# Kernel optimization log

Measured on AMD Instinct MI355X. Metric: run time of the kernel, lower is better.

Reference implementation:

```python
import jax, jax.numpy as jnp
import numpy as np

# MSDeformAttn-style fusion config (canonical deformable-DETR defaults)
D = 256      # d_model
NH = 8       # n_heads
NP = 4       # n_points per level
NL = 2       # n_levels (= num_feature_levels: modality v and modality i)
B, H, W = 4, 64, 64


def setup_inputs() -> dict:
    key = jax.random.key(0)
    ks = jax.random.split(key, 8)
    s = 0.02
    return {
        'input_v': jax.random.normal(ks[0], (B, D, H, W), jnp.float32),
        'input_i': jax.random.normal(ks[1], (B, D, H, W), jnp.float32),
        'W_value': jax.random.normal(ks[2], (D, D), jnp.float32) * s,
        'b_value': jnp.zeros((D,), jnp.float32),
        'W_off':   jax.random.normal(ks[3], (D, NH * NL * NP * 2), jnp.float32) * s,
        'b_off':   jax.random.normal(ks[4], (NH * NL * NP * 2,), jnp.float32) * s,
        'W_attn':  jax.random.normal(ks[5], (D, NH * NL * NP), jnp.float32) * s,
        'b_attn':  jnp.zeros((NH * NL * NP,), jnp.float32),
        'W_out':   jax.random.normal(ks[6], (D, D), jnp.float32) * s,
        'b_out':   jnp.zeros((D,), jnp.float32),
    }


def _bilinear_sample(value_l, locs, Hl, Wl):
    # value_l: (B, NH, HW, dh)  flattened per-level value
    # locs:    (B, Lq, NH, NP, 2) normalized sampling locations in [0,1]
    # returns  (B, NH, Lq, NP, dh); grid_sample semantics: zeros padding, align_corners=False
    b, nh, hw, dh = value_l.shape
    lq = locs.shape[1]
    x = locs[..., 0] * Wl - 0.5
    y = locs[..., 1] * Hl - 0.5
    x0 = jnp.floor(x)
    y0 = jnp.floor(y)
    dx = x - x0
    dy = y - y0
    x0i = x0.astype(jnp.int32)
    y0i = y0.astype(jnp.int32)
    out = jnp.zeros((b, nh, lq, NP, dh), value_l.dtype)
    corners = [
        (x0i,     y0i,     (1 - dx) * (1 - dy)),
        (x0i + 1, y0i,     dx * (1 - dy)),
        (x0i,     y0i + 1, (1 - dx) * dy),
        (x0i + 1, y0i + 1, dx * dy),
    ]
    for xi, yi, wgt in corners:
        valid = ((xi >= 0) & (xi < Wl) & (yi >= 0) & (yi < Hl)).astype(value_l.dtype)
        idx = jnp.clip(yi, 0, Hl - 1) * Wl + jnp.clip(xi, 0, Wl - 1)      # (B,Lq,NH,NP)
        idx_t = idx.transpose(0, 2, 1, 3).reshape(b, nh, lq * NP, 1)       # (B,NH,Lq*NP,1)
        g = jnp.take_along_axis(value_l, idx_t, axis=2)                    # (B,NH,Lq*NP,dh)
        g = g.reshape(b, nh, lq, NP, dh)
        w_t = (wgt * valid).transpose(0, 2, 1, 3)[..., None]               # (B,NH,Lq,NP,1)
        out = out + g * w_t
    return out


def reference(input_v, input_i, W_value, b_value, W_off, b_off, W_attn, b_attn, W_out, b_out):
    b, c, h, w = input_v.shape
    hw = h * w
    lq = NL * hw
    dh = c // NH

    # flatten both modalities into one token sequence (level 0 = v, level 1 = i)
    src_v = input_v.reshape(b, c, hw).transpose(0, 2, 1)
    src_i = input_i.reshape(b, c, hw).transpose(0, 2, 1)
    src = jnp.concatenate([src_v, src_i], axis=1)                          # (B, Lq, C)

    value = (src @ W_value + b_value).reshape(b, lq, NH, dh)
    value = value.transpose(0, 2, 1, 3)                                    # (B, NH, Lq, dh)
    value_levels = [value[:, :, :hw], value[:, :, hw:]]

    offsets = (src @ W_off + b_off).reshape(b, lq, NH, NL, NP, 2)
    attn = jax.nn.softmax((src @ W_attn + b_attn).reshape(b, lq, NH, NL * NP), axis=-1)
    attn = attn.reshape(b, lq, NH, NL, NP)

    # reference points: normalized pixel centers, same grid for both levels
    xs = (jnp.arange(w, dtype=jnp.float32) + 0.5) / w
    ys = (jnp.arange(h, dtype=jnp.float32) + 0.5) / h
    gy, gx = jnp.meshgrid(ys, xs, indexing='ij')
    ref = jnp.stack([gx.reshape(-1), gy.reshape(-1)], axis=-1)             # (HW, 2)
    ref = jnp.concatenate([ref, ref], axis=0)                              # (Lq, 2)

    norm = jnp.array([w, h], dtype=jnp.float32)
    locs = ref[None, :, None, None, None, :] + offsets / norm              # (B,Lq,NH,NL,NP,2)

    sampled = jnp.stack(
        [_bilinear_sample(value_levels[l], locs[:, :, :, l], h, w) for l in range(NL)],
        axis=3)                                                            # (B,NH,Lq,NL,NP,dh)

    fused = jnp.einsum('bqhlp,bhqlpd->bqhd', attn, sampled).reshape(b, lq, c)
    out = fused @ W_out + b_out                                            # (B, Lq, C)

    out_v = out[:, :hw]
    out_i = out[:, hw:]
    o = out_v + out_i                                                      # (B, HW, C)
    return o.transpose(0, 2, 1).reshape(b, c, h, w)
```

## Files before the change

### kernel.cpp

```cpp
#include <hip/hip_runtime.h>

#define HW 4096
#define LQ 8192
#define DD 256

typedef __bf16 bf16x8 __attribute__((ext_vector_type(8)));
typedef float  f32x4  __attribute__((ext_vector_type(4)));
typedef unsigned int u32;
typedef u32 u32x4 __attribute__((ext_vector_type(4)));
typedef u32 u32x2 __attribute__((ext_vector_type(2)));

__device__ __forceinline__ float bflo(u32 u) { return __uint_as_float(u << 16); }
__device__ __forceinline__ float bfhi(u32 u) { return __uint_as_float(u & 0xffff0000u); }

#define GLOAD16(g, l) __builtin_amdgcn_global_load_lds(                     \
    (__attribute__((address_space(1))) void*)(g),                          \
    (__attribute__((address_space(3))) void*)(l), 16, 0, 0)

__global__ __launch_bounds__(256) void prep_all(const float* __restrict__ in_v,
                                                const float* __restrict__ in_i,
                                                const float* __restrict__ Wv,
                                                const float* __restrict__ Wo,
                                                const float* __restrict__ Wa,
                                                const float* __restrict__ Wout,
                                                char* __restrict__ srcS,
                                                char* __restrict__ WcatT,
                                                char* __restrict__ WoutT)
{
    __shared__ float tile[64][68];
    if (blockIdx.z < 8) {
        const int q0 = blockIdx.x * 64;
        const int k0 = blockIdx.y * 64;
        const int bz = blockIdx.z;
        const float* src = ((bz & 1) ? in_i : in_v) + (size_t)(bz >> 1) * (DD * HW);
        const int t  = threadIdx.x;
        const int ql = (t & 15) * 4;
        const int kl = t >> 4;
#pragma unroll
        for (int rr = 0; rr < 4; ++rr) {
            const float4 v = *(const float4*)(src + (size_t)(k0 + kl + rr * 16) * HW + q0 + ql);
            *(float4*)&tile[kl + rr * 16][ql] = v;
        }
        __syncthreads();
        const int qrow = t >> 2;
        const int kc   = (t & 3) * 16;
        const int row  = (bz >> 1) * LQ + (bz & 1) * HW + q0 + qrow;
        bf16x8 p0, p1;
#pragma unroll
        for (int j = 0; j < 8; ++j) {
            p0[j] = (__bf16)tile[kc + j][qrow];
            p1[j] = (__bf16)tile[kc + 8 + j][qrow];
        }
        char* drow = srcS + (size_t)row * 512;
        const int sw   = (row & 7) << 4;
        const int base = k0 * 2 + kc * 2;
        *(bf16x8*)(drow + ((base)      ^ sw)) = p0;
        *(bf16x8*)(drow + ((base + 16) ^ sw)) = p1;
    } else {
        const int flat = blockIdx.y * 64 + blockIdx.x;
        if (flat >= 120) return;
        const int gi = flat * 256 + threadIdx.x;
        if (gi < 448 * 32) {
            const int row = gi >> 5;
            const int g   = gi & 31;
            const int k   = g * 8;
            const float* col; int stride;
            if (row < 256)      { col = Wv + row;         stride = 256; }
            else if (row < 384) { col = Wo + (row - 256); stride = 128; }
            else                { col = Wa + (row - 384); stride = 64;  }
            bf16x8 p;
#pragma unroll
            for (int j = 0; j < 8; ++j) p[j] = (__bf16)col[(size_t)(k + j) * stride];
            char* d = WcatT + (size_t)row * 512;
            *(bf16x8*)(d + ((g * 16) ^ ((row & 7) << 4))) = p;
        } else {
            const int gj = gi - 448 * 32;
            if (gj >= 256 * 64) return;
            const int c = gj >> 6;
            const int g = gj & 63;
            const int k = (g * 8) & 255;
            bf16x8 p;
#pragma unroll
            for (int j = 0; j < 8; ++j) p[j] = (__bf16)Wout[(size_t)(k + j) * 256 + c];
            char* d = WoutT + (size_t)c * 1024;
            *(bf16x8*)(d + ((g * 16) ^ ((c & 7) << 4))) = p;
        }
    }
}

__global__ __launch_bounds__(256) void mfma_proj(const char* __restrict__ srcS,
                                                 const char* __restrict__ WcatT,
                                                 const float* __restrict__ b_value,
                                                 const float* __restrict__ b_off,
                                                 const float* __restrict__ b_attn,
                                                 __bf16* __restrict__ valueB,
                                                 __bf16* __restrict__ offB,
                                                 __bf16* __restrict__ attnB)
{
    __shared__ char smem[24576];
    char* As = smem;
    char* Bs = smem + 16384;

    const int M0 = blockIdx.x * 128;
    const int N0 = blockIdx.y * 64;
    const int t = threadIdx.x;
    const int w = t >> 6;
    const int l = t & 63;
    const int lm = l & 15, lk = l >> 4;
    const int wave_m = (w >> 1) * 64;
    const int wave_n = (w & 1) * 32;

    f32x4 acc[4][2] = {};

    const char* Ab = As + (wave_m + lm) * 128;
    const char* Bb = Bs + (wave_n + lm) * 128;
    const int go0 = (lk ^ (l & 7)) * 16;
    const int go1 = go0 ^ 64;

    for (int kt = 0; kt < 4; ++kt) {
        __syncthreads();
        const int kb = kt * 128;
#pragma unroll
        for (int c = 0; c < 4; ++c) {
            const char* g = srcS + (size_t)(M0 + w * 32 + c * 8 + (l >> 3)) * 512 + kb + (l & 7) * 16;
            GLOAD16(g, As + (w * 4 + c) * 1024);
        }
#pragma unroll
        for (int c = 0; c < 2; ++c) {
            const char* g = WcatT + (size_t)(N0 + w * 16 + c * 8 + (l >> 3)) * 512 + kb + (l & 7) * 16;
            GLOAD16(g, Bs + (w * 2 + c) * 1024);
        }
        __syncthreads();

        bf16x8 af[4], bb[2];
#pragma unroll
        for (int mi = 0; mi < 4; ++mi) af[mi] = *(const bf16x8*)(Ab + mi * 2048 + go0);
#pragma unroll
        for (int ni = 0; ni < 2; ++ni) bb[ni] = *(const bf16x8*)(Bb + ni * 2048 + go0);
#pragma unroll
        for (int mi = 0; mi < 4; ++mi)
#pragma unroll
            for (int ni = 0; ni < 2; ++ni)
                acc[mi][ni] = __builtin_amdgcn_mfma_f32_16x16x32_bf16(af[mi], bb[ni], acc[mi][ni], 0, 0, 0);
#pragma unroll
        for (int mi = 0; mi < 4; ++mi) af[mi] = *(const bf16x8*)(Ab + mi * 2048 + go1);
#pragma unroll
        for (int ni = 0; ni < 2; ++ni) bb[ni] = *(const bf16x8*)(Bb + ni * 2048 + go1);
#pragma unroll
        for (int mi = 0; mi < 4; ++mi)
#pragma unroll
            for (int ni = 0; ni < 2; ++ni)
                acc[mi][ni] = __builtin_amdgcn_mfma_f32_16x16x32_bf16(af[mi], bb[ni], acc[mi][ni], 0, 0, 0);
    }

    if (N0 < 256) {
#pragma unroll
        for (int ni = 0; ni < 2; ++ni) {
            const int cl = N0 + wave_n + ni * 16 + lm;
            const float bv = b_value[cl];
#pragma unroll
            for (int mi = 0; mi < 4; ++mi) {
                const int row = M0 + wave_m + mi * 16 + lk * 4;
#pragma unroll
                for (int r = 0; r < 4; ++r)
                    valueB[(size_t)(row + r) * 256 + cl] = (__bf16)(acc[mi][ni][r] + bv);
            }
        }
    } else if (N0 < 384) {
#pragma unroll
        for (int ni = 0; ni < 2; ++ni) {
            const int cl = (N0 - 256) + wave_n + ni * 16 + lm;
            const float bv = b_off[cl];
#pragma unroll
            for (int mi = 0; mi < 4; ++mi) {
                const int row = M0 + wave_m + mi * 16 + lk * 4;
#pragma unroll
                for (int r = 0; r < 4; ++r)
                    offB[(size_t)(row + r) * 128 + cl] = (__bf16)(acc[mi][ni][r] + bv);
            }
        }
    } else {
#pragma unroll
        for (int ni = 0; ni < 2; ++ni) {
            const int cl = wave_n + ni * 16 + lm;
            const float bv = b_attn[cl];
#pragma unroll
            for (int mi = 0; mi < 4; ++mi) {
                const int row = M0 + wave_m + mi * 16 + lk * 4;
#pragma unroll
                for (int r = 0; r < 4; ++r)
                    attnB[(size_t)(row + r) * 64 + cl] = (__bf16)(acc[mi][ni][r] + bv);
            }
        }
    }
}

__global__ __launch_bounds__(256) void sample_kernel(const char* __restrict__ valueB,
                                                     const char* __restrict__ offB,
                                                     const char* __restrict__ attnB,
                                                     char* __restrict__ fusedS)
{
    __shared__ u32 wlds[4][128][8];
    const int bid0 = blockIdx.x;
    const int bid  = ((bid0 & 7) << 9) | (bid0 >> 3);
    const int w    = threadIdx.x >> 6;
    const int lane = threadIdx.x & 63;
    const int q2   = lane >> 5;
    const int sub  = lane & 31;
    const int head = sub >> 2;
    const int dl   = sub & 3;

    const int px   = bid & 15;
    const int py   = (bid >> 4) & 31;
    const int half = (bid >> 9) & 1;
    const int b    = bid >> 10;
    const int x    = px * 4 + (w & 1) * 2 + q2;
    const int y    = py * 2 + (w >> 1);
    const int row  = b * LQ + half * HW + y * 64 + x;
    const float fx0 = (float)x;
    const float fy0 = (float)y;

    const u32x4 lgp = *(const u32x4*)(attnB + (size_t)row * 128 + head * 16);
    float e8[8];
#pragma unroll
    for (int j = 0; j < 4; ++j) { e8[2 * j] = bflo(lgp[j]); e8[2 * j + 1] = bfhi(lgp[j]); }
    float mx = e8[0];
#pragma unroll
    for (int j = 1; j < 8; ++j) mx = fmaxf(mx, e8[j]);
    const int pt0 = dl * 2;
    const float ex0 = __expf(e8[pt0] - mx);
    const float ex1 = __expf(e8[pt0 + 1] - mx);
    float sp = ex0 + ex1;
    sp += __shfl_xor(sp, 1);
    sp += __shfl_xor(sp, 2);
    const float inv = 1.0f / sp;

    const u32x2 opk = *(const u32x2*)(offB + (size_t)row * 256 + head * 32 + dl * 8);
    u32* slotp = &wlds[w][q2 * 64 + head * 8 + pt0][0];
#pragma unroll
    for (int i = 0; i < 2; ++i) {
        const float ox = bflo(opk[i]);
        const float oy = bfhi(opk[i]);
        const float aw = (i ? ex1 : ex0) * inv;
        const float xx = fx0 + ox;
        const float yy = fy0 + oy;
        const float xf = floorf(xx), yf = floorf(yy);
        const int   xi = (int)xf,   yi = (int)yf;
        const float dx = xx - xf,   dy = yy - yf;
        const bool vx0 = (unsigned)xi       < 64u;
        const bool vx1 = (unsigned)(xi + 1) < 64u;
        const bool vy0 = (unsigned)yi       < 64u;
        const bool vy1 = (unsigned)(yi + 1) < 64u;
        f32x4 W;
        W[0] = (vx0 && vy0) ? aw * (1.f - dx) * (1.f - dy) : 0.f;
        W[1] = (vx1 && vy0) ? aw * dx * (1.f - dy)         : 0.f;
        W[2] = (vx0 && vy1) ? aw * (1.f - dx) * dy         : 0.f;
        W[3] = (vx1 && vy1) ? aw * dx * dy                 : 0.f;
        const int xc0 = min(max(xi, 0), 63);
        const int xc1 = min(max(xi + 1, 0), 63);
        const int yc0 = min(max(yi, 0), 63) << 6;
        const int yc1 = min(max(yi + 1, 0), 63) << 6;
        const int lvl = ((pt0 + i) >> 2) * HW;
        u32x4 S;
        S[0] = lvl + yc0 + xc0; S[1] = lvl + yc0 + xc1;
        S[2] = lvl + yc1 + xc0; S[3] = lvl + yc1 + xc1;
        *(f32x4*)(slotp + i * 8)     = W;
        *(u32x4*)(slotp + i * 8 + 4) = S;
    }

    const int d8 = dl << 3;
    const char* vb = valueB + (((size_t)(b * LQ)) << 9) + head * 64 + d8 * 2;
    const u32* slotb = &wlds[w][q2 * 64 + head * 8][0];
    float acc[8] = {};
    __builtin_amdgcn_s_setprio(1);
#pragma unroll
    for (int pt = 0; pt < 8; ++pt) {
        const f32x4 W = *(const f32x4*)(slotb + pt * 8);
        const u32x4 S = *(const u32x4*)(slotb + pt * 8 + 4);
        const u32x4 g00 = *(const u32x4*)(vb + ((size_t)S[0] << 9));
        const u32x4 g10 = *(const u32x4*)(vb + ((size_t)S[1] << 9));
        const u32x4 g01 = *(const u32x4*)(vb + ((size_t)S[2] << 9));
        const u32x4 g11 = *(const u32x4*)(vb + ((size_t)S[3] << 9));
#pragma unroll
        for (int j = 0; j < 4; ++j) {
            acc[2 * j]     += W[0] * bflo(g00[j]) + W[1] * bflo(g10[j]) + W[2] * bflo(g01[j]) + W[3] * bflo(g11[j]);
            acc[2 * j + 1] += W[0] * bfhi(g00[j]) + W[1] * bfhi(g10[j]) + W[2] * bfhi(g01[j]) + W[3] * bfhi(g11[j]);
        }
    }
    __builtin_amdgcn_s_setprio(0);

    bf16x8 ov;
#pragma unroll
    for (int j = 0; j < 8; ++j) ov[j] = (__bf16)acc[j];
    const int bo = (head * 64 + d8 * 2) ^ ((row & 7) << 4);
    *(bf16x8*)(fusedS + (size_t)row * 512 + bo) = ov;
}

__global__ __launch_bounds__(256) void mfma_out(const char* __restrict__ fusedS,
                                                const char* __restrict__ WoutT,
                                                const float* __restrict__ b_out,
                                                float* __restrict__ out)
{
    __shared__ char smem[24576];
    char* As = smem;
    char* Bs = smem + 16384;
    float* Tr = (float*)smem;

    const int M0 = blockIdx.x * 128;
    const int N0 = blockIdx.y * 64;
    const int bi = M0 >> 12;
    const int q0 = M0 & 4095;
    const int t = threadIdx.x;
    const int w = t >> 6;
    const int l = t & 63;
    const int lm = l & 15, lk = l >> 4;
    const int wave_m = (w >> 1) * 64;
    const int wave_n = (w & 1) * 32;

    f32x4 acc[4][2] = {};

    const char* Ab = As + (wave_m + lm) * 128;
    const char* Bb = Bs + (wave_n + lm) * 128;
    const int go0 = (lk ^ (l & 7)) * 16;
    const int go1 = go0 ^ 64;

    for (int kt = 0; kt < 8; ++kt) {
        __syncthreads();
        const int half = kt >> 2;
        const int kb   = (kt & 3) * 128;
#pragma unroll
        for (int c = 0; c < 4; ++c) {
            const char* g = fusedS + (size_t)(bi * LQ + half * HW + q0 + w * 32 + c * 8 + (l >> 3)) * 512
                          + kb + (l & 7) * 16;
            GLOAD16(g, As + (w * 4 + c) * 1024);
        }
#pragma unroll
        for (int c = 0; c < 2; ++c) {
            const char* g = WoutT + (size_t)(N0 + w * 16 + c * 8 + (l >> 3)) * 1024 + kt * 128 + (l & 7) * 16;
            GLOAD16(g, Bs + (w * 2 + c) * 1024);
        }
        __syncthreads();

        bf16x8 af[4], bb[2];
#pragma unroll
        for (int mi = 0; mi < 4; ++mi) af[mi] = *(const bf16x8*)(Ab + mi * 2048 + go0);
#pragma unroll
        for (int ni = 0; ni < 2; ++ni) bb[ni] = *(const bf16x8*)(Bb + ni * 2048 + go0);
#pragma unroll
        for (int mi = 0; mi < 4; ++mi)
#pragma unroll
            for (int ni = 0; ni < 2; ++ni)
                acc[mi][ni] = __builtin_amdgcn_mfma_f32_16x16x32_bf16(af[mi], bb[ni], acc[mi][ni], 0, 0, 0);
#pragma unroll
        for (int mi = 0; mi < 4; ++mi) af[mi] = *(const bf16x8*)(Ab + mi * 2048 + go1);
#pragma unroll
        for (int ni = 0; ni < 2; ++ni) bb[ni] = *(const bf16x8*)(Bb + ni * 2048 + go1);
#pragma unroll
        for (int mi = 0; mi < 4; ++mi)
#pragma unroll
            for (int ni = 0; ni < 2; ++ni)
                acc[mi][ni] = __builtin_amdgcn_mfma_f32_16x16x32_bf16(af[mi], bb[ni], acc[mi][ni], 0, 0, 0);
    }

    float bias2[2];
#pragma unroll
    for (int ni = 0; ni < 2; ++ni) bias2[ni] = 2.0f * b_out[N0 + wave_n + ni * 16 + lm];

#pragma unroll
    for (int h = 0; h < 2; ++h) {
        __syncthreads();
        if ((w >> 1) == h) {
#pragma unroll
            for (int mi = 0; mi < 4; ++mi)
#pragma unroll
                for (int ni = 0; ni < 2; ++ni)
#pragma unroll
                    for (int r = 0; r < 4; ++r)
                        Tr[(wave_n + ni * 16 + lm) * 68 + mi * 16 + lk * 4 + r] = acc[mi][ni][r] + bias2[ni];
        }
        __syncthreads();
        const int c  = t >> 2;
        const int qo = (t & 3) * 16;
        float* dst = out + ((size_t)(bi * DD + N0 + c)) * HW + q0 + h * 64 + qo;
        const float* sp = Tr + c * 68 + qo;
#pragma unroll
        for (int j = 0; j < 4; ++j)
            *(f32x4*)(dst + j * 4) = *(const f32x4*)(sp + j * 4);
    }
}

extern "C" void kernel_launch(void* const* d_in, const int* in_sizes, int n_in,
                              void* d_out, int out_size, void* d_ws, size_t ws_size,
                              hipStream_t stream) {
    const float* in_v    = (const float*)d_in[0];
    const float* in_i    = (const float*)d_in[1];
    const float* W_value = (const float*)d_in[2];
    const float* b_value = (const float*)d_in[3];
    const float* W_off   = (const float*)d_in[4];
    const float* b_off   = (const float*)d_in[5];
    const float* W_attn  = (const float*)d_in[6];
    const float* b_attn  = (const float*)d_in[7];
    const float* W_out   = (const float*)d_in[8];
    const float* b_out   = (const float*)d_in[9];
    float* out = (float*)d_out;

    char* ws = (char*)d_ws;
    __bf16* valueB = (__bf16*)(ws);
    __bf16* offB   = (__bf16*)(ws + 16777216);
    __bf16* attnB  = (__bf16*)(ws + 25165824);
    char*   srcS   = ws + 29360128;
    char*   fusedS = ws + 46137344;
    char*   WcatT  = ws + 62914560;
    char*   WoutT  = ws + 63143936;

    prep_all<<<dim3(64, 4, 9), 256, 0, stream>>>(in_v, in_i, W_value, W_off, W_attn, W_out,
                                                 srcS, WcatT, WoutT);
    mfma_proj<<<dim3(256, 7), 256, 0, stream>>>(srcS, WcatT, b_value, b_off, b_attn,
                                                valueB, offB, attnB);
    sample_kernel<<<dim3(4096), 256, 0, stream>>>((const char*)valueB, (const char*)offB,
                                                  (const char*)attnB, fusedS);
    mfma_out<<<dim3(128, 4), 256, 0, stream>>>(fusedS, WoutT, b_out, out);
}
```

Before: 76.80 us.

## Widen projection GEMM N-tile to 128 and pack bilinear accumulation into float2

The projection GEMM now uses 128-wide N tiles for the value and offset columns (a 64-wide tile only for the attention logits), so the grid goes from 7 to 4 column blocks. Each A tile is then loaded fewer times, and shared memory grows to 32KB. The sampling kernel stores pre-shifted byte offsets in LDS, removing per-gather shifts and 64-bit address math. It also accumulates bilinear results as float2 vectors, which may let the compiler emit packed FMA instructions. The larger tile raises register and LDS use per block and may lower occupancy.

```diff
diff --git a/kernel.cpp b/kernel.cpp
--- a/kernel.cpp
+++ b/kernel.cpp
@@ -6,6 +6,7 @@
 
 typedef __bf16 bf16x8 __attribute__((ext_vector_type(8)));
 typedef float  f32x4  __attribute__((ext_vector_type(4)));
+typedef float  f32x2  __attribute__((ext_vector_type(2)));
 typedef unsigned int u32;
 typedef u32 u32x4 __attribute__((ext_vector_type(4)));
 typedef u32 u32x2 __attribute__((ext_vector_type(2)));
@@ -88,6 +89,91 @@
     }
 }
 
+template<int BN>
+__device__ __forceinline__ void proj_tile(char* smem,
+                                          const char* __restrict__ srcS,
+                                          const char* __restrict__ WcatT,
+                                          const float* __restrict__ b_value,
+                                          const float* __restrict__ b_off,
+                                          const float* __restrict__ b_attn,
+                                          __bf16* __restrict__ valueB,
+                                          __bf16* __restrict__ offB,
+                                          __bf16* __restrict__ attnB,
+                                          int M0, int N0)
+{
+    constexpr int NI = BN / 32;
+    char* As = smem;
+    char* Bs = smem + 16384;
+
+    const int t = threadIdx.x;
+    const int w = t >> 6;
+    const int l = t & 63;
+    const int lm = l & 15, lk = l >> 4;
+    const int wave_m = (w >> 1) * 64;
+    const int wave_n = (w & 1) * (BN / 2);
+
+    f32x4 acc[4][NI] = {};
+
+    const char* Ab = As + (wave_m + lm) * 128;
+    const char* Bb = Bs + (wave_n + lm) * 128;
+    const int go0 = (lk ^ (l & 7)) * 16;
+    const int go1 = go0 ^ 64;
+
+    for (int kt = 0; kt < 4; ++kt) {
+        __syncthreads();
+        const int kb = kt * 128;
+#pragma unroll
+        for (int c = 0; c < 4; ++c) {
+            const char* g = srcS + (size_t)(M0 + w * 32 + c * 8 + (l >> 3)) * 512 + kb + (l & 7) * 16;
+            GLOAD16(g, As + (w * 4 + c) * 1024);
+        }
+#pragma unroll
+        for (int c = 0; c < NI; ++c) {
+            const char* g = WcatT + (size_t)(N0 + w * (BN / 4) + c * 8 + (l >> 3)) * 512 + kb + (l & 7) * 16;
+            GLOAD16(g, Bs + (w * NI + c) * 1024);
+        }
+        __syncthreads();
+
+        bf16x8 af[4], bb[NI];
+#pragma unroll
+        for (int mi = 0; mi < 4; ++mi) af[mi] = *(const bf16x8*)(Ab + mi * 2048 + go0);
+#pragma unroll
+        for (int ni = 0; ni < NI; ++ni) bb[ni] = *(const bf16x8*)(Bb + ni * 2048 + go0);
+#pragma unroll
+        for (int mi = 0; mi < 4; ++mi)
+#pragma unroll
+            for (int ni = 0; ni < NI; ++ni)
+                acc[mi][ni] = __builtin_amdgcn_mfma_f32_16x16x32_bf16(af[mi], bb[ni], acc[mi][ni], 0, 0, 0);
+#pragma unroll
+        for (int mi = 0; mi < 4; ++mi) af[mi] = *(const bf16x8*)(Ab + mi * 2048 + go1);
+#pragma unroll
+        for (int ni = 0; ni < NI; ++ni) bb[ni] = *(const bf16x8*)(Bb + ni * 2048 + go1);
+#pragma unroll
+        for (int mi = 0; mi < 4; ++mi)
+#pragma unroll
+            for (int ni = 0; ni < NI; ++ni)
+                acc[mi][ni] = __builtin_amdgcn_mfma_f32_16x16x32_bf16(af[mi], bb[ni], acc[mi][ni], 0, 0, 0);
+    }
+
+    __bf16* outp; const float* bias; int ncols, nbase;
+    if (N0 < 256)       { outp = valueB; bias = b_value; ncols = 256; nbase = 0;   }
+    else if (N0 < 384)  { outp = offB;   bias = b_off;   ncols = 128; nbase = 256; }
+    else                { outp = attnB;  bias = b_attn;  ncols = 64;  nbase = 384; }
+
+#pragma unroll
+    for (int ni = 0; ni < NI; ++ni) {
+        const int cl = N0 + wave_n + ni * 16 + lm - nbase;
+        const float bv = bias[cl];
+#pragma unroll
+        for (int mi = 0; mi < 4; ++mi) {
+            const int row = M0 + wave_m + mi * 16 + lk * 4;
+#pragma unroll
+            for (int r = 0; r < 4; ++r)
+                outp[(size_t)(row + r) * ncols + cl] = (__bf16)(acc[mi][ni][r] + bv);
+        }
+    }
+}
+
 __global__ __launch_bounds__(256) void mfma_proj(const char* __restrict__ srcS,
                                                  const char* __restrict__ WcatT,
                                                  const float* __restrict__ b_value,
@@ -97,102 +183,14 @@
                                                  __bf16* __restrict__ offB,
                                                  __bf16* __restrict__ attnB)
 {
-    __shared__ char smem[24576];
-    char* As = smem;
-    char* Bs = smem + 16384;
-
+    __shared__ char smem[32768];
     const int M0 = blockIdx.x * 128;
-    const int N0 = blockIdx.y * 64;
-    const int t = threadIdx.x;
-    const int w = t >> 6;
-    const int l = t & 63;
-    const int lm = l & 15, lk = l >> 4;
-    const int wave_m = (w >> 1) * 64;
-    const int wave_n = (w & 1) * 32;
-
-    f32x4 acc[4][2] = {};
-
-    const char* Ab = As + (wave_m + lm) * 128;
-    const char* Bb = Bs + (wave_n + lm) * 128;
-    const int go0 = (lk ^ (l & 7)) * 16;
-    const int go1 = go0 ^ 64;
-
-    for (int kt = 0; kt < 4; ++kt) {
-        __syncthreads();
-        const int kb = kt * 128;
-#pragma unroll
-        for (int c = 0; c < 4; ++c) {
-            const char* g = srcS + (size_t)(M0 + w * 32 + c * 8 + (l >> 3)) * 512 + kb + (l & 7) * 16;
-            GLOAD16(g, As + (w * 4 + c) * 1024);
-        }
-#pragma unroll
-        for (int c = 0; c < 2; ++c) {
-            const char* g = WcatT + (size_t)(N0 + w * 16 + c * 8 + (l >> 3)) * 512 + kb + (l & 7) * 16;
-            GLOAD16(g, Bs + (w * 2 + c) * 1024);
-        }
-        __syncthreads();
-
-        bf16x8 af[4], bb[2];
-#pragma unroll
-        for (int mi = 0; mi < 4; ++mi) af[mi] = *(const bf16x8*)(Ab + mi * 2048 + go0);
-#pragma unroll
-        for (int ni = 0; ni < 2; ++ni) bb[ni] = *(const bf16x8*)(Bb + ni * 2048 + go0);
-#pragma unroll
-        for (int mi = 0; mi < 4; ++mi)
-#pragma unroll
-            for (int ni = 0; ni < 2; ++ni)
-                acc[mi][ni] = __builtin_amdgcn_mfma_f32_16x16x32_bf16(af[mi], bb[ni], acc[mi][ni], 0, 0, 0);
-#pragma unroll
-        for (int mi = 0; mi < 4; ++mi) af[mi] = *(const bf16x8*)(Ab + mi * 2048 + go1);
-#pragma unroll
-        for (int ni = 0; ni < 2; ++ni) bb[ni] = *(const bf16x8*)(Bb + ni * 2048 + go1);
-#pragma unroll
-        for (int mi = 0; mi < 4; ++mi)
-#pragma unroll
-            for (int ni = 0; ni < 2; ++ni)
-                acc[mi][ni] = __builtin_amdgcn_mfma_f32_16x16x32_bf16(af[mi], bb[ni], acc[mi][ni], 0, 0, 0);
-    }
-
-    if (N0 < 256) {
-#pragma unroll
-        for (int ni = 0; ni < 2; ++ni) {
-            const int cl = N0 + wave_n + ni * 16 + lm;
-            const float bv = b_value[cl];
-#pragma unroll
-            for (int mi = 0; mi < 4; ++mi) {
-                const int row = M0 + wave_m + mi * 16 + lk * 4;
-#pragma unroll
-                for (int r = 0; r < 4; ++r)
-                    valueB[(size_t)(row + r) * 256 + cl] = (__bf16)(acc[mi][ni][r] + bv);
-            }
-        }
-    } else if (N0 < 384) {
-#pragma unroll
-        for (int ni = 0; ni < 2; ++ni) {
-            const int cl = (N0 - 256) + wave_n + ni * 16 + lm;
-            const float bv = b_off[cl];
-#pragma unroll
-            for (int mi = 0; mi < 4; ++mi) {
-                const int row = M0 + wave_m + mi * 16 + lk * 4;
-#pragma unroll
-                for (int r = 0; r < 4; ++r)
-                    offB[(size_t)(row + r) * 128 + cl] = (__bf16)(acc[mi][ni][r] + bv);
-            }
-        }
-    } else {
-#pragma unroll
-        for (int ni = 0; ni < 2; ++ni) {
-            const int cl = wave_n + ni * 16 + lm;
-            const float bv = b_attn[cl];
-#pragma unroll
-            for (int mi = 0; mi < 4; ++mi) {
-                const int row = M0 + wave_m + mi * 16 + lk * 4;
-#pragma unroll
-                for (int r = 0; r < 4; ++r)
-                    attnB[(size_t)(row + r) * 64 + cl] = (__bf16)(acc[mi][ni][r] + bv);
-            }
-        }
-    }
+    if (blockIdx.y < 3)
+        proj_tile<128>(smem, srcS, WcatT, b_value, b_off, b_attn,
+                       valueB, offB, attnB, M0, blockIdx.y * 128);
+    else
+        proj_tile<64>(smem, srcS, WcatT, b_value, b_off, b_attn,
+                      valueB, offB, attnB, M0, 384);
 }
 
 __global__ __launch_bounds__(256) void sample_kernel(const char* __restrict__ valueB,
@@ -262,8 +260,8 @@
         const int yc1 = min(max(yi + 1, 0), 63) << 6;
         const int lvl = ((pt0 + i) >> 2) * HW;
         u32x4 S;
-        S[0] = lvl + yc0 + xc0; S[1] = lvl + yc0 + xc1;
-        S[2] = lvl + yc1 + xc0; S[3] = lvl + yc1 + xc1;
+        S[0] = (u32)(lvl + yc0 + xc0) << 9; S[1] = (u32)(lvl + yc0 + xc1) << 9;
+        S[2] = (u32)(lvl + yc1 + xc0) << 9; S[3] = (u32)(lvl + yc1 + xc1) << 9;
         *(f32x4*)(slotp + i * 8)     = W;
         *(u32x4*)(slotp + i * 8 + 4) = S;
     }
@@ -271,27 +269,37 @@
     const int d8 = dl << 3;
     const char* vb = valueB + (((size_t)(b * LQ)) << 9) + head * 64 + d8 * 2;
     const u32* slotb = &wlds[w][q2 * 64 + head * 8][0];
-    float acc[8] = {};
+    f32x2 acc2[4] = {};
     __builtin_amdgcn_s_setprio(1);
 #pragma unroll
     for (int pt = 0; pt < 8; ++pt) {
         const f32x4 W = *(const f32x4*)(slotb + pt * 8);
         const u32x4 S = *(const u32x4*)(slotb + pt * 8 + 4);
-        const u32x4 g00 = *(const u32x4*)(vb + ((size_t)S[0] << 9));
-        const u32x4 g10 = *(const u32x4*)(vb + ((size_t)S[1] << 9));
-        const u32x4 g01 = *(const u32x4*)(vb + ((size_t)S[2] << 9));
-        const u32x4 g11 = *(const u32x4*)(vb + ((size_t)S[3] << 9));
+        const u32x4 g00 = *(const u32x4*)(vb + S[0]);
+        const u32x4 g10 = *(const u32x4*)(vb + S[1]);
+        const u32x4 g01 = *(const u32x4*)(vb + S[2]);
+        const u32x4 g11 = *(const u32x4*)(vb + S[3]);
+        const f32x2 w0 = {W[0], W[0]};
+        const f32x2 w1 = {W[1], W[1]};
+        const f32x2 w2 = {W[2], W[2]};
+        const f32x2 w3 = {W[3], W[3]};
 #pragma unroll
         for (int j = 0; j < 4; ++j) {
-            acc[2 * j]     += W[0] * bflo(g00[j]) + W[1] * bflo(g10[j]) + W[2] * bflo(g01[j]) + W[3] * bflo(g11[j]);
-            acc[2 * j + 1] += W[0] * bfhi(g00[j]) + W[1] * bfhi(g10[j]) + W[2] * bfhi(g01[j]) + W[3] * bfhi(g11[j]);
+            const f32x2 v00 = {bflo(g00[j]), bfhi(g00[j])};
+            const f32x2 v10 = {bflo(g10[j]), bfhi(g10[j])};
+            const f32x2 v01 = {bflo(g01[j]), bfhi(g01[j])};
+            const f32x2 v11 = {bflo(g11[j]), bfhi(g11[j])};
+            acc2[j] += w0 * v00 + w1 * v10 + w2 * v01 + w3 * v11;
         }
     }
     __builtin_amdgcn_s_setprio(0);
 
     bf16x8 ov;
 #pragma unroll
-    for (int j = 0; j < 8; ++j) ov[j] = (__bf16)acc[j];
+    for (int j = 0; j < 4; ++j) {
+        ov[2 * j]     = (__bf16)acc2[j][0];
+        ov[2 * j + 1] = (__bf16)acc2[j][1];
+    }
     const int bo = (head * 64 + d8 * 2) ^ ((row & 7) << 4);
     *(bf16x8*)(fusedS + (size_t)row * 512 + bo) = ov;
 }
@@ -415,7 +423,7 @@
 
     prep_all<<<dim3(64, 4, 9), 256, 0, stream>>>(in_v, in_i, W_value, W_off, W_attn, W_out,
                                                  srcS, WcatT, WoutT);
-    mfma_proj<<<dim3(256, 7), 256, 0, stream>>>(srcS, WcatT, b_value, b_off, b_attn,
+    mfma_proj<<<dim3(256, 4), 256, 0, stream>>>(srcS, WcatT, b_value, b_off, b_attn,
                                                 valueB, offB, attnB);
     sample_kernel<<<dim3(4096), 256, 0, stream>>>((const char*)valueB, (const char*)offB,
                                                   (const char*)attnB, fusedS);
```

Result: faster. 72.80 us, median of 3 (-5.2%).
